# Performance work log

Measured on AMD Instinct MI355X. Metric: run time of the kernel, lower is better.

## Reference

```python
import jax, jax.numpy as jnp
import numpy as np

N_NODES = 50000
D = 128
N_EDGES = 800000


def _gcn_layer(h, W, b, row, col, mask, n_nodes):
    # Linear: h @ W.T + b  (nn.Linear convention)
    h = h @ W.T + b
    # degree of source nodes, counting only non-self-loop edges (remove_self_loops)
    deg = jax.ops.segment_sum(mask.astype(h.dtype), row, num_segments=n_nodes)
    deg_inv_sqrt = jnp.where(deg > 0, jax.lax.rsqrt(jnp.maximum(deg, 1.0)), 0.0)
    norm = deg_inv_sqrt[row] * deg_inv_sqrt[col] * mask.astype(h.dtype)
    # gather-scale messages [E, D], scatter-add into target nodes (col)
    msg = norm[:, None] * h[row]
    return jax.ops.segment_sum(msg, col, num_segments=n_nodes)


def setup_inputs() -> dict:
    key = jax.random.key(0)
    ks = jax.random.split(key, 9)
    x = jax.random.normal(ks[0], (N_NODES, D), dtype=jnp.float32)
    edge_index = jax.random.randint(ks[1], (2, N_EDGES), 0, N_NODES, dtype=jnp.int64)
    lim = 1.0 / np.sqrt(D)
    params = {}
    for i in range(3):
        params[f"W{i}"] = jax.random.uniform(ks[2 + 2 * i], (D, D), jnp.float32, -lim, lim)
        params[f"b{i}"] = jax.random.uniform(ks[3 + 2 * i], (D,), jnp.float32, -lim, lim)
    return {"x": x, "edge_index": edge_index, **params}


def reference(x, edge_index, W0, b0, W1, b1, W2, b2):
    row, col = edge_index[0], edge_index[1]
    mask = row != col  # remove_self_loops
    h = x
    for W, b in ((W0, b0), (W1, b1), (W2, b2)):
        h_new = jax.nn.relu(_gcn_layer(h, W, b, row, col, mask, x.shape[0]))
        h = h + h_new
    return h
```

## Files before the change

kernel.cpp:

```cpp
#include <hip/hip_runtime.h>
#include <hip/hip_bf16.h>


#define D_DIM 128
#define SCAN_CHUNK 1024
#define CHUNKS 256
#define GROUPS 8
#define GS (CHUNKS / GROUPS)
#define LDSW 12512

typedef __attribute__((ext_vector_type(8))) short bf16x8;
typedef __attribute__((ext_vector_type(4))) float f32x4;

static __device__ __forceinline__ short f2bf(float f) {
    union { __hip_bfloat16 b; short s; } u;
    u.b = __float2bfloat16(f);
    return u.s;
}
static __device__ __forceinline__ float bf_lo(unsigned p) { return __uint_as_float(p << 16); }
static __device__ __forceinline__ float bf_hi(unsigned p) { return __uint_as_float(p & 0xffff0000u); }


__global__ __launch_bounds__(256) void hist_kernel(const int* __restrict__ ei,
                                                   unsigned* __restrict__ partial_col,
                                                   unsigned* __restrict__ partial_row,
                                                   const float* __restrict__ W0,
                                                   const float* __restrict__ W1,
                                                   const float* __restrict__ W2,
                                                   unsigned short* __restrict__ Wb,
                                                   int E, int CHSZ) {
    int tid = threadIdx.x;
    if (blockIdx.y == 2) {
        int i = blockIdx.x * 256 + tid;
        if (i < 3 * D_DIM * D_DIM) {
            const float* W = (i < 16384) ? W0 : (i < 32768) ? W1 : W2;
            Wb[i] = (unsigned short)f2bf(W[i & 16383]);
        }
        return;
    }
    __shared__ unsigned hh[LDSW];
    int ch = blockIdx.x;
    int docol = (blockIdx.y == 0);
    for (int i = tid; i < LDSW; i += 256) hh[i] = 0u;
    __syncthreads();
    int e0 = ch * CHSZ, e1 = min(e0 + CHSZ, E);
    for (int e = e0 + tid; e < e1; e += 256) {
        int row = ei[e];
        int col = ei[E + e];
        if (row == col) continue;
        int bin = docol ? col : row;
        atomicAdd(&hh[bin >> 2], 1u << ((bin & 3) * 8));
    }
    __syncthreads();
    unsigned* dst = (docol ? partial_col : partial_row) + (size_t)ch * LDSW;
    for (int i = tid; i < LDSW; i += 256) dst[i] = hh[i];
}

__global__ __launch_bounds__(256) void group_prefix_kernel(
    unsigned* __restrict__ partial_col, const unsigned* __restrict__ partial_row,
    unsigned* __restrict__ gsum_col, unsigned* __restrict__ gsum_row, int NW) {
    int w = blockIdx.x * 256 + threadIdx.x;
    if (w >= NW) return;
    int g = blockIdx.y;
    size_t base = (size_t)(g * GS) * LDSW + w;
    if (blockIdx.z == 0) {
        unsigned run = 0;
#pragma unroll 4
        for (int c = 0; c < GS; c++) {
            unsigned v = partial_col[base + (size_t)c * LDSW];
            partial_col[base + (size_t)c * LDSW] = run;
            run += v;
        }
        gsum_col[g * NW + w] = run;
    } else {
        unsigned run = 0;
#pragma unroll 4
        for (int c = 0; c < GS; c++) run += partial_row[base + (size_t)c * LDSW];
        gsum_row[g * NW + w] = run;
    }
}

__global__ __launch_bounds__(256) void cnt_dis_kernel(
    unsigned* __restrict__ gsum_col, const unsigned* __restrict__ gsum_row,
    int* __restrict__ col_cnt, float* __restrict__ dis, int* __restrict__ bsum, int NW) {
    __shared__ int wsum[4];
    int w = blockIdx.x * 256 + threadIdx.x;
    int s = 0;
    if (w < NW) {
        unsigned wcv[GROUPS];
        unsigned clo = 0, chi = 0, rlo = 0, rhi = 0;
#pragma unroll
        for (int g = 0; g < GROUPS; g++) {
            unsigned wc = gsum_col[g * NW + w];
            unsigned wr = gsum_row[g * NW + w];
            wcv[g] = wc;
            clo += wc & 0x00FF00FFu; chi += (wc >> 8) & 0x00FF00FFu;
            rlo += wr & 0x00FF00FFu; rhi += (wr >> 8) & 0x00FF00FFu;
        }
        unsigned run = 0;
#pragma unroll
        for (int g = 0; g < GROUPS; g++) {
            gsum_col[g * NW + w] = run;
            run += wcv[g];
        }
        int c0 = clo & 0xFFFF, c1 = chi & 0xFFFF, c2 = clo >> 16, c3 = chi >> 16;
        int r0 = rlo & 0xFFFF, r1 = rhi & 0xFFFF, r2 = rlo >> 16, r3 = rhi >> 16;
        ((int4*)col_cnt)[w] = make_int4(c0, c1, c2, c3);
        float4 dv;
        dv.x = (r0 > 0) ? rsqrtf((float)r0) : 0.0f;
        dv.y = (r1 > 0) ? rsqrtf((float)r1) : 0.0f;
        dv.z = (r2 > 0) ? rsqrtf((float)r2) : 0.0f;
        dv.w = (r3 > 0) ? rsqrtf((float)r3) : 0.0f;
        ((float4*)dis)[w] = dv;
        s = c0 + c1 + c2 + c3;
    }
#pragma unroll
    for (int d = 32; d > 0; d >>= 1) s += __shfl_down(s, d, 64);
    int lane = threadIdx.x & 63, wv = threadIdx.x >> 6;
    if (lane == 0) wsum[wv] = s;
    __syncthreads();
    if (threadIdx.x == 0) bsum[blockIdx.x] = wsum[0] + wsum[1] + wsum[2] + wsum[3];
}

__global__ __launch_bounds__(256) void scan_final_kernel(const int* __restrict__ cnt,
                                                         const int* __restrict__ bsum,
                                                         int* __restrict__ offs,
                                                         int n, int G) {
    __shared__ int wsum[4];
    __shared__ int sblock;
    int base = blockIdx.x * SCAN_CHUNK;
    int tid = threadIdx.x;
    const int PT = SCAN_CHUNK / 256;
    int v[PT];
    int s = 0;
#pragma unroll
    for (int i = 0; i < PT; i++) {
        int g = base + tid * PT + i;
        v[i] = (g < n) ? cnt[g] : 0;
        s += v[i];
    }
    int local_sum = s;
    int lane = tid & 63, w = tid >> 6;
#pragma unroll
    for (int d = 1; d < 64; d <<= 1) {
        int t = __shfl_up(s, d, 64);
        if (lane >= d) s += t;
    }
    if (lane == 63) wsum[w] = s;
    if (tid < 64) {
        int bv = (tid < G) ? bsum[tid] : 0;
        int bs = bv;
#pragma unroll
        for (int d = 1; d < 64; d <<= 1) {
            int t = __shfl_up(bs, d, 64);
            if (tid >= d) bs += t;
        }
        if (tid == blockIdx.x) sblock = bs - bv;
        if (tid == 63 && blockIdx.x == G - 1) offs[n] = bs;
    }
    __syncthreads();
    int wbase = 0;
    for (int i = 0; i < w; i++) wbase += wsum[i];
    int run = sblock + wbase + (s - local_sum);
#pragma unroll
    for (int i = 0; i < PT; i++) {
        int g = base + tid * PT + i;
        if (g < n) offs[g] = run;
        run += v[i];
    }
}

__global__ __launch_bounds__(256) void scatter_kernel(const int* __restrict__ ei,
                                                      const float* __restrict__ dis,
                                                      const int* __restrict__ offs,
                                                      const unsigned* __restrict__ chpref,
                                                      const unsigned* __restrict__ gpref,
                                                      unsigned* __restrict__ epack,
                                                      int E, int CHSZ, int NW) {
    __shared__ unsigned cur[LDSW];
    int tid = threadIdx.x;
    int ch = blockIdx.x;
    const unsigned* pf = chpref + (size_t)ch * LDSW;
    const unsigned* gb = gpref + (size_t)(ch / GS) * NW;
    for (int i = tid; i < LDSW; i += 256) {
        unsigned seed = pf[i];
        if (i < NW) seed += gb[i];
        cur[i] = seed;
    }
    __syncthreads();
    int e0 = ch * CHSZ, e1 = min(e0 + CHSZ, E);
    for (int e = e0 + tid; e < e1; e += 256) {
        int row = ei[e];
        int col = ei[E + e];
        if (row == col) continue;
        float wgt = dis[row] * dis[col];
        int wd = col >> 2, sh = (col & 3) * 8;
        unsigned old = atomicAdd(&cur[wd], 1u << sh);
        int slot = offs[col] + (int)((old >> sh) & 0xFFu);
        epack[slot] = (unsigned)row | ((unsigned)(unsigned short)f2bf(wgt) << 16);
    }
}


__global__ __launch_bounds__(256) void linear_mfma_kernel(
    const float* __restrict__ A, const unsigned short* __restrict__ Wb,
    const float* __restrict__ bias, unsigned short* __restrict__ hWb, int nrows) {
    __shared__ unsigned short stage[4][16 * 136];
    int wave = threadIdx.x >> 6;
    int lane = threadIdx.x & 63;
    int r0 = blockIdx.x * 64 + wave * 16;
    int m = lane & 15, q = lane >> 4;
    int rload = min(r0 + m, nrows - 1);
    const float4* h4 = (const float4*)A;

    f32x4 acc[8];
#pragma unroll
    for (int jt = 0; jt < 8; jt++) acc[jt] = (f32x4){0.f, 0.f, 0.f, 0.f};

#pragma unroll
    for (int k0 = 0; k0 < 128; k0 += 32) {
        int c0 = k0 + q * 8;
        float4 x0 = h4[rload * 32 + (c0 >> 2)];
        float4 x1 = h4[rload * 32 + (c0 >> 2) + 1];
        bf16x8 a;
        a[0] = f2bf(x0.x); a[1] = f2bf(x0.y); a[2] = f2bf(x0.z); a[3] = f2bf(x0.w);
        a[4] = f2bf(x1.x); a[5] = f2bf(x1.y); a[6] = f2bf(x1.z); a[7] = f2bf(x1.w);
#pragma unroll
        for (int jt = 0; jt < 8; jt++) {
            bf16x8 b = *(const bf16x8*)(Wb + (jt * 16 + m) * D_DIM + c0);
            acc[jt] = __builtin_amdgcn_mfma_f32_16x16x32_bf16(a, b, acc[jt], 0, 0, 0);
        }
    }

#pragma unroll
    for (int jt = 0; jt < 8; jt++) {
        float bv = bias[jt * 16 + m];
#pragma unroll
        for (int reg = 0; reg < 4; reg++)
            stage[wave][(q * 4 + reg) * 136 + jt * 16 + m] =
                (unsigned short)f2bf(acc[jt][reg] + bv);
    }
#pragma unroll
    for (int t = 0; t < 4; t++) {
        int rl = t * 4 + (lane >> 4);
        int gr = r0 + rl;
        if (gr < nrows) {
            uint4 v = *(const uint4*)&stage[wave][rl * 136 + (lane & 15) * 8];
            *(uint4*)&hWb[(size_t)gr * D_DIM + (lane & 15) * 8] = v;
        }
    }
}

__global__ __launch_bounds__(256) void agg_kernel(const int* __restrict__ offs,
                                                  const unsigned* __restrict__ epack,
                                                  const uint4* __restrict__ hW4,
                                                  const float* __restrict__ hprev,
                                                  float* __restrict__ hout, int n_nodes) {
    int node = (int)((blockIdx.x * blockDim.x + threadIdx.x) >> 6);
    int lane = threadIdx.x & 63;
    if (node >= n_nodes) return;
    int g = lane >> 4, s = lane & 15;

    int beg = offs[node];
    int end = offs[node + 1];

    float acc[8];
#pragma unroll
    for (int k = 0; k < 8; k++) acc[k] = 0.f;

    for (int i = beg; i < end; i += 16) {
        int last = end - 1;
        int i0 = i + g, i1 = i0 + 4, i2 = i0 + 8, i3 = i0 + 12;
        unsigned e0 = epack[min(i0, last)];
        unsigned e1 = epack[min(i1, last)];
        unsigned e2 = epack[min(i2, last)];
        unsigned e3 = epack[min(i3, last)];
        uint4 p0 = hW4[(e0 & 0xffffu) * 16 + s];
        uint4 p1 = hW4[(e1 & 0xffffu) * 16 + s];
        uint4 p2 = hW4[(e2 & 0xffffu) * 16 + s];
        uint4 p3 = hW4[(e3 & 0xffffu) * 16 + s];
        float w0 = (i0 < end) ? bf_hi(e0) : 0.f;
        float w1 = (i1 < end) ? bf_hi(e1) : 0.f;
        float w2 = (i2 < end) ? bf_hi(e2) : 0.f;
        float w3 = (i3 < end) ? bf_hi(e3) : 0.f;
        acc[0] = fmaf(w0, bf_lo(p0.x), acc[0]); acc[1] = fmaf(w0, bf_hi(p0.x), acc[1]);
        acc[2] = fmaf(w0, bf_lo(p0.y), acc[2]); acc[3] = fmaf(w0, bf_hi(p0.y), acc[3]);
        acc[4] = fmaf(w0, bf_lo(p0.z), acc[4]); acc[5] = fmaf(w0, bf_hi(p0.z), acc[5]);
        acc[6] = fmaf(w0, bf_lo(p0.w), acc[6]); acc[7] = fmaf(w0, bf_hi(p0.w), acc[7]);
        acc[0] = fmaf(w1, bf_lo(p1.x), acc[0]); acc[1] = fmaf(w1, bf_hi(p1.x), acc[1]);
        acc[2] = fmaf(w1, bf_lo(p1.y), acc[2]); acc[3] = fmaf(w1, bf_hi(p1.y), acc[3]);
        acc[4] = fmaf(w1, bf_lo(p1.z), acc[4]); acc[5] = fmaf(w1, bf_hi(p1.z), acc[5]);
        acc[6] = fmaf(w1, bf_lo(p1.w), acc[6]); acc[7] = fmaf(w1, bf_hi(p1.w), acc[7]);
        acc[0] = fmaf(w2, bf_lo(p2.x), acc[0]); acc[1] = fmaf(w2, bf_hi(p2.x), acc[1]);
        acc[2] = fmaf(w2, bf_lo(p2.y), acc[2]); acc[3] = fmaf(w2, bf_hi(p2.y), acc[3]);
        acc[4] = fmaf(w2, bf_lo(p2.z), acc[4]); acc[5] = fmaf(w2, bf_hi(p2.z), acc[5]);
        acc[6] = fmaf(w2, bf_lo(p2.w), acc[6]); acc[7] = fmaf(w2, bf_hi(p2.w), acc[7]);
        acc[0] = fmaf(w3, bf_lo(p3.x), acc[0]); acc[1] = fmaf(w3, bf_hi(p3.x), acc[1]);
        acc[2] = fmaf(w3, bf_lo(p3.y), acc[2]); acc[3] = fmaf(w3, bf_hi(p3.y), acc[3]);
        acc[4] = fmaf(w3, bf_lo(p3.z), acc[4]); acc[5] = fmaf(w3, bf_hi(p3.z), acc[5]);
        acc[6] = fmaf(w3, bf_lo(p3.w), acc[6]); acc[7] = fmaf(w3, bf_hi(p3.w), acc[7]);
    }

#pragma unroll
    for (int k = 0; k < 8; k++) {
        acc[k] += __shfl_xor(acc[k], 16, 64);
        acc[k] += __shfl_xor(acc[k], 32, 64);
    }

    if (g == 0) {
        const float4* hp4 = (const float4*)hprev;
        float4* ho4 = (float4*)hout;
        int idx = node * 32 + s * 2;
        float4 h0 = hp4[idx], h1 = hp4[idx + 1];
        float4 o0, o1;
        o0.x = h0.x + fmaxf(acc[0], 0.f); o0.y = h0.y + fmaxf(acc[1], 0.f);
        o0.z = h0.z + fmaxf(acc[2], 0.f); o0.w = h0.w + fmaxf(acc[3], 0.f);
        o1.x = h1.x + fmaxf(acc[4], 0.f); o1.y = h1.y + fmaxf(acc[5], 0.f);
        o1.z = h1.z + fmaxf(acc[6], 0.f); o1.w = h1.w + fmaxf(acc[7], 0.f);
        ho4[idx] = o0;
        ho4[idx + 1] = o1;
    }
}


static inline size_t align_up(size_t x, size_t a) { return (x + a - 1) & ~(a - 1); }

extern "C" void kernel_launch(void* const* d_in, const int* in_sizes, int n_in,
                              void* d_out, int out_size, void* d_ws, size_t ws_size,
                              hipStream_t stream) {
    const float* x = (const float*)d_in[0];
    const int* ei = (const int*)d_in[1];
    const float* Wl[3] = {(const float*)d_in[2], (const float*)d_in[4], (const float*)d_in[6]};
    const float* bl[3] = {(const float*)d_in[3], (const float*)d_in[5], (const float*)d_in[7]};

    const int N = in_sizes[0] / D_DIM;
    const int E = in_sizes[1] / 2;
    const int NW = N / 4;
    const int G = (N + SCAN_CHUNK - 1) / SCAN_CHUNK;
    const int NWB = (NW + 255) / 256;
    const int CHSZ = (E + CHUNKS - 1) / CHUNKS;

    char* p = (char*)d_ws;
    int* col_cnt = (int*)p;            p += align_up((size_t)N * 4, 256);
    int* offs    = (int*)p;            p += align_up((size_t)(N + 1) * 4, 256);
    float* dis   = (float*)p;          p += align_up((size_t)N * 4, 256);
    int* bsum    = (int*)p;            p += align_up((size_t)64 * 4, 256);
    unsigned* partial_col = (unsigned*)p;  p += align_up((size_t)CHUNKS * LDSW * 4, 256);
    unsigned* partial_row = (unsigned*)p;  p += align_up((size_t)CHUNKS * LDSW * 4, 256);
    unsigned* gsum_col = (unsigned*)p; p += align_up((size_t)GROUPS * NW * 4, 256);
    unsigned* gsum_row = (unsigned*)p; p += align_up((size_t)GROUPS * NW * 4, 256);
    unsigned short* Wb = (unsigned short*)p;  p += align_up((size_t)3 * D_DIM * D_DIM * 2, 256);
    unsigned* epack = (unsigned*)p;    p += align_up((size_t)E * 4, 256);
    unsigned short* hWb = (unsigned short*)p;  p += align_up((size_t)N * D_DIM * 2, 256);
    (void)ws_size;

    hist_kernel<<<dim3(CHUNKS, 3), 256, 0, stream>>>(ei, partial_col, partial_row,
                                                     Wl[0], Wl[1], Wl[2], Wb, E, CHSZ);
    group_prefix_kernel<<<dim3(NWB, GROUPS, 2), 256, 0, stream>>>(partial_col, partial_row,
                                                                  gsum_col, gsum_row, NW);
    cnt_dis_kernel<<<NWB, 256, 0, stream>>>(gsum_col, gsum_row, col_cnt, dis, bsum, NW);
    scan_final_kernel<<<G, 256, 0, stream>>>(col_cnt, bsum, offs, N, G);
    scatter_kernel<<<CHUNKS, 256, 0, stream>>>(ei, dis, offs, partial_col, gsum_col,
                                               epack, E, CHSZ, NW);

    const float* hprev = x;
    float* h = (float*)d_out;
    int gemm_blocks = (N + 63) / 64;
    int agg_blocks = (N + 3) / 4;
    for (int l = 0; l < 3; l++) {
        linear_mfma_kernel<<<gemm_blocks, 256, 0, stream>>>(hprev, Wb + l * 16384, bl[l], hWb, N);
        agg_kernel<<<agg_blocks, 256, 0, stream>>>(offs, epack, (const uint4*)hWb, hprev, h, N);
        hprev = h;
    }
}
```

Before: 302.0 us.

## Fuse first-layer linear GEMM into histogram kernel launch

Adds a fourth grid slice to the histogram kernel that computes the layer-0 linear transform (x @ W0.T + b0) with bf16 MFMA, reading fp32 weights directly and converting on the fly. The separate layer-0 GEMM launch is removed, so that GEMM runs alongside the edge histogramming instead of after the CSR build. The histogram grid grows to cover the GEMM blocks, so extra blocks in the histogram slices exit early. This saves one launch and overlaps independent work, at the cost of redundant per-block weight conversion and heavier blocks sharing the launch.

```diff
diff --git a/kernel.cpp b/kernel.cpp
--- a/kernel.cpp
+++ b/kernel.cpp
@@ -28,7 +28,11 @@
                                                    const float* __restrict__ W1,
                                                    const float* __restrict__ W2,
                                                    unsigned short* __restrict__ Wb,
-                                                   int E, int CHSZ) {
+                                                   const float* __restrict__ x,
+                                                   const float* __restrict__ b0,
+                                                   unsigned short* __restrict__ hWb,
+                                                   int nrows, int E, int CHSZ) {
+    __shared__ unsigned hh[LDSW];
     int tid = threadIdx.x;
     if (blockIdx.y == 2) {
         int i = blockIdx.x * 256 + tid;
@@ -38,8 +42,60 @@
         }
         return;
     }
-    __shared__ unsigned hh[LDSW];
+    if (blockIdx.y == 3) {
+        int wave = tid >> 6;
+        int lane = tid & 63;
+        int r0 = blockIdx.x * 64 + wave * 16;
+        if (r0 >= nrows) return;
+        int m = lane & 15, q = lane >> 4;
+        int rload = min(r0 + m, nrows - 1);
+        const float4* h4 = (const float4*)x;
+        const float4* w4 = (const float4*)W0;
+
+        f32x4 acc[8];
+#pragma unroll
+        for (int jt = 0; jt < 8; jt++) acc[jt] = (f32x4){0.f, 0.f, 0.f, 0.f};
+
+#pragma unroll
+        for (int k0 = 0; k0 < 128; k0 += 32) {
+            int c0 = k0 + q * 8;
+            float4 x0 = h4[rload * 32 + (c0 >> 2)];
+            float4 x1 = h4[rload * 32 + (c0 >> 2) + 1];
+            bf16x8 a;
+            a[0] = f2bf(x0.x); a[1] = f2bf(x0.y); a[2] = f2bf(x0.z); a[3] = f2bf(x0.w);
+            a[4] = f2bf(x1.x); a[5] = f2bf(x1.y); a[6] = f2bf(x1.z); a[7] = f2bf(x1.w);
+#pragma unroll
+            for (int jt = 0; jt < 8; jt++) {
+                float4 w0v = w4[(jt * 16 + m) * 32 + (c0 >> 2)];
+                float4 w1v = w4[(jt * 16 + m) * 32 + (c0 >> 2) + 1];
+                bf16x8 b;
+                b[0] = f2bf(w0v.x); b[1] = f2bf(w0v.y); b[2] = f2bf(w0v.z); b[3] = f2bf(w0v.w);
+                b[4] = f2bf(w1v.x); b[5] = f2bf(w1v.y); b[6] = f2bf(w1v.z); b[7] = f2bf(w1v.w);
+                acc[jt] = __builtin_amdgcn_mfma_f32_16x16x32_bf16(a, b, acc[jt], 0, 0, 0);
+            }
+        }
+        unsigned short* stg = (unsigned short*)hh + wave * 16 * 136;
+#pragma unroll
+        for (int jt = 0; jt < 8; jt++) {
+            float bv = b0[jt * 16 + m];
+#pragma unroll
+            for (int reg = 0; reg < 4; reg++)
+                stg[(q * 4 + reg) * 136 + jt * 16 + m] =
+                    (unsigned short)f2bf(acc[jt][reg] + bv);
+        }
+#pragma unroll
+        for (int t = 0; t < 4; t++) {
+            int rl = t * 4 + (lane >> 4);
+            int gr = r0 + rl;
+            if (gr < nrows) {
+                uint4 v = *(const uint4*)&stg[rl * 136 + (lane & 15) * 8];
+                *(uint4*)&hWb[(size_t)gr * D_DIM + (lane & 15) * 8] = v;
+            }
+        }
+        return;
+    }
     int ch = blockIdx.x;
+    if (ch >= CHUNKS) return;
     int docol = (blockIdx.y == 0);
     for (int i = tid; i < LDSW; i += 256) hh[i] = 0u;
     __syncthreads();
@@ -354,8 +410,12 @@
     unsigned short* hWb = (unsigned short*)p;  p += align_up((size_t)N * D_DIM * 2, 256);
     (void)ws_size;
 
-    hist_kernel<<<dim3(CHUNKS, 3), 256, 0, stream>>>(ei, partial_col, partial_row,
-                                                     Wl[0], Wl[1], Wl[2], Wb, E, CHSZ);
+    int gemm_blocks = (N + 63) / 64;
+    int hist_gx = (gemm_blocks > CHUNKS) ? gemm_blocks : CHUNKS;
+
+    hist_kernel<<<dim3(hist_gx, 4), 256, 0, stream>>>(ei, partial_col, partial_row,
+                                                      Wl[0], Wl[1], Wl[2], Wb,
+                                                      x, bl[0], hWb, N, E, CHSZ);
     group_prefix_kernel<<<dim3(NWB, GROUPS, 2), 256, 0, stream>>>(partial_col, partial_row,
                                                                   gsum_col, gsum_row, NW);
     cnt_dis_kernel<<<NWB, 256, 0, stream>>>(gsum_col, gsum_row, col_cnt, dis, bsum, NW);
@@ -365,10 +425,11 @@
 
     const float* hprev = x;
     float* h = (float*)d_out;
-    int gemm_blocks = (N + 63) / 64;
     int agg_blocks = (N + 3) / 4;
     for (int l = 0; l < 3; l++) {
-        linear_mfma_kernel<<<gemm_blocks, 256, 0, stream>>>(hprev, Wb + l * 16384, bl[l], hWb, N);
+        if (l > 0)
+            linear_mfma_kernel<<<gemm_blocks, 256, 0, stream>>>(hprev, Wb + l * 16384,
+                                                                bl[l], hWb, N);
         agg_kernel<<<agg_blocks, 256, 0, stream>>>(offs, epack, (const uint4*)hWb, hprev, h, N);
         hprev = h;
     }
```

Result: slower. 308.2 us (+2.1%).
